# Performance work log

Measured on AMD Instinct MI355X. Metric: run time of the kernel, lower is better.

## Reference

```python
import jax, jax.numpy as jnp
import numpy as np

DIM, FF, E = 1024, 4096, 8
B, S = 2, 2048


def setup_inputs() -> dict:
    key = jax.random.key(0)
    ks = jax.random.split(key, 7)
    sd = 0.02
    return {
        "x":  jax.random.normal(ks[0], (B, S, DIM), dtype=jnp.float32),
        "Wg": jax.random.normal(ks[1], (DIM, E), dtype=jnp.float32) * sd,
        "bg": jnp.zeros((E,), dtype=jnp.float32),
        "W1": jax.random.normal(ks[2], (E, DIM, FF), dtype=jnp.float32) * sd,
        "b1": jnp.zeros((E, FF), dtype=jnp.float32),
        "W2": jax.random.normal(ks[3], (E, FF, DIM), dtype=jnp.float32) * sd,
        "b2": jnp.zeros((E, DIM), dtype=jnp.float32),
    }


def reference(x, Wg, bg, W1, b1, W2, b2):
    # Gate: (B,S,E) softmax over experts
    probs = jax.nn.softmax(x @ Wg + bg, axis=-1)
    # Dense all-expert FFN (matches torch.stack over all experts), dropout is identity (eval)
    h = jax.nn.relu(jnp.einsum("bsd,edf->bsef", x, W1) + b1)        # (B,S,E,FF)
    all_out = jnp.einsum("bsef,efd->bsed", h, W2) + b2               # (B,S,E,DIM)
    # Top-2 routing, renormalized weights
    top_vals, top_idx = jax.lax.top_k(probs, 2)                      # (B,S,2)
    weights = top_vals / (jnp.sum(top_vals, axis=-1, keepdims=True) + 1e-9)
    selected = jnp.take_along_axis(all_out, top_idx[..., None], axis=2)  # (B,S,2,DIM)
    return jnp.sum(selected * weights[..., None], axis=2)            # (B,S,DIM)
```

## Files before the change

kernel.cpp:

```cpp
#include <hip/hip_runtime.h>
#include <hip/hip_bf16.h>


typedef __attribute__((ext_vector_type(8))) short bf16x8;
typedef __attribute__((ext_vector_type(4))) float f32x4;

#define MFMA16(a, b, c) __builtin_amdgcn_mfma_f32_16x16x32_bf16((a), (b), (c), 0, 0, 0)

__device__ __forceinline__ unsigned short f2bf(float f) {
  unsigned u = __builtin_bit_cast(unsigned, f);
  u += 0x7FFFu + ((u >> 16) & 1u);
  return (unsigned short)(u >> 16);
}

__device__ __forceinline__ float bf2f(unsigned short s) {
  return __builtin_bit_cast(float, (unsigned)s << 16);
}

__device__ __forceinline__ void gload_lds16(const void* g, void* l) {
  __builtin_amdgcn_global_load_lds(
      (const __attribute__((address_space(1))) unsigned int*)g,
      (__attribute__((address_space(3))) unsigned int*)l, 16, 0, 0);
}

__device__ __forceinline__ bf16x8 ldsr128(const void* p) {
  bf16x8 r;
  unsigned a = (unsigned)(unsigned long long)p;
  asm volatile("ds_read_b128 %0, %1" : "=v"(r) : "v"(a));
  return r;
}

__global__ __launch_bounds__(256) void gate_kernel(
    const float* __restrict__ x, const float* __restrict__ Wg,
    const float* __restrict__ bg, int* __restrict__ tok_e,
    float* __restrict__ tok_w, unsigned short* __restrict__ xb) {
  const int wave = threadIdx.x >> 6;
  const int lane = threadIdx.x & 63;
  const int t = blockIdx.x * 4 + wave;
  const float* xr = x + (size_t)t * 1024;
  unsigned short* xrow = xb + (size_t)t * 1024;
  double acc[8] = {0, 0, 0, 0, 0, 0, 0, 0};
  for (int i = 0; i < 16; ++i) {
    const int d = i * 64 + lane;
    const float vx = xr[d];
    xrow[d] = f2bf(vx);
    const double xv = (double)vx;
    const float* wr = Wg + d * 8;
#pragma unroll
    for (int e = 0; e < 8; ++e) acc[e] += xv * (double)wr[e];
  }
#pragma unroll
  for (int e = 0; e < 8; ++e) {
    double v = acc[e];
#pragma unroll
    for (int off = 32; off > 0; off >>= 1) v += __shfl_xor(v, off, 64);
    acc[e] = v + (double)bg[e];
  }
  if (lane == 0) {
    int e0 = 0;
#pragma unroll
    for (int e = 1; e < 8; ++e)
      if (acc[e] > acc[e0]) e0 = e;
    int e1 = (e0 == 0) ? 1 : 0;
#pragma unroll
    for (int e = 0; e < 8; ++e) {
      if (e != e0 && acc[e] > acc[e1]) e1 = e;
    }
    const double m = acc[e0];
    double s = 0.0;
#pragma unroll
    for (int e = 0; e < 8; ++e) s += exp(acc[e] - m);
    const double p0 = exp(acc[e0] - m) / s;
    const double p1 = exp(acc[e1] - m) / s;
    const double den = p0 + p1 + 1e-9;
    tok_e[2 * t] = e0;
    tok_e[2 * t + 1] = e1;
    tok_w[2 * t] = (float)(p0 / den);
    tok_w[2 * t + 1] = (float)(p1 / den);
  }
}

__global__ __launch_bounds__(256) void scan_scatter_kernel(
    const int* __restrict__ tok_e, int* __restrict__ counts,
    int* __restrict__ offsets, int* __restrict__ pair_token,
    int* __restrict__ tok_slot) {
  __shared__ int scnt[8];
  __shared__ int scur[8];
  const int tid = threadIdx.x;
  if (tid < 8) scnt[tid] = 0;
  __syncthreads();
  for (int i = tid; i < 8192; i += 256) atomicAdd(&scnt[tok_e[i]], 1);
  __syncthreads();
  if (tid == 0) {
    int s = 0;
    for (int e = 0; e < 8; ++e) {
      counts[e] = scnt[e];
      offsets[e] = s;
      scur[e] = s;
      s += scnt[e];
    }
  }
  __syncthreads();
  for (int t = tid; t < 4096; t += 256) {
#pragma unroll
    for (int j = 0; j < 2; ++j) {
      const int e = tok_e[2 * t + j];
      const int slot = atomicAdd(&scur[e], 1);
      pair_token[slot] = t;
      tok_slot[2 * t + j] = slot;
    }
  }
}

__global__ __launch_bounds__(256) void transW_kernel(
    const float* __restrict__ W1, const float* __restrict__ W2,
    unsigned short* __restrict__ W1t, unsigned short* __restrict__ W2t, int FC,
    int f0, int nW1) {
  __shared__ __align__(16) unsigned short T[64][520];
  const int tid = threadIdx.x;
  const int qi = (tid & 15) * 4;
  const int qo = (tid >> 4) * 4;

  const float* src;
  size_t srcStride;
  unsigned short* dstBase;
  size_t dstStride;

  const int bid = blockIdx.x;
  if (bid < nW1) {
    const int nf = FC / 64;
    const int e = bid / (2 * nf);
    const int rem = bid % (2 * nf);
    const int fb = (rem % nf) * 64;
    const int kb = (rem / nf) * 512;
    src = W1 + ((size_t)e * 1024 + kb) * 4096 + f0 + fb + qi;
    srcStride = 4096;
    dstBase = W1t + ((size_t)e * FC + fb) * 1024 + kb;
    dstStride = 1024;
  } else {
    const int jd = bid - nW1;
    const int nf = FC / 512;
    const int e = jd / (16 * nf);
    const int rem = jd % (16 * nf);
    const int db = (rem % 16) * 64;
    const int fbl = (rem / 16) * 512;
    src = W2 + ((size_t)e * 4096 + f0 + fbl) * 1024 + db + qi;
    srcStride = 1024;
    dstBase = W2t + ((size_t)e * 1024 + db) * FC + fbl;
    dstStride = FC;
  }

#pragma unroll
  for (int it = 0; it < 8; ++it) {
    const int o0 = it * 64 + qo;
    const float* s = src + (size_t)o0 * srcStride;
    const float4 r0 = *(const float4*)s;
    const float4 r1 = *(const float4*)(s + srcStride);
    const float4 r2 = *(const float4*)(s + 2 * srcStride);
    const float4 r3 = *(const float4*)(s + 3 * srcStride);
    uint2 u;
    u.x = (unsigned)f2bf(r0.x) | ((unsigned)f2bf(r1.x) << 16);
    u.y = (unsigned)f2bf(r2.x) | ((unsigned)f2bf(r3.x) << 16);
    *(uint2*)&T[qi + 0][o0] = u;
    u.x = (unsigned)f2bf(r0.y) | ((unsigned)f2bf(r1.y) << 16);
    u.y = (unsigned)f2bf(r2.y) | ((unsigned)f2bf(r3.y) << 16);
    *(uint2*)&T[qi + 1][o0] = u;
    u.x = (unsigned)f2bf(r0.z) | ((unsigned)f2bf(r1.z) << 16);
    u.y = (unsigned)f2bf(r2.z) | ((unsigned)f2bf(r3.z) << 16);
    *(uint2*)&T[qi + 2][o0] = u;
    u.x = (unsigned)f2bf(r0.w) | ((unsigned)f2bf(r1.w) << 16);
    u.y = (unsigned)f2bf(r2.w) | ((unsigned)f2bf(r3.w) << 16);
    *(uint2*)&T[qi + 3][o0] = u;
  }
  __syncthreads();
  const int rr = tid >> 2;
  const int sg = tid & 3;
  unsigned short* dst = dstBase + (size_t)rr * dstStride;
#pragma unroll
  for (int j = 0; j < 16; ++j) {
    const int c = sg + j * 4;
    *(uint4*)(dst + c * 8) = *(const uint4*)&T[rr][c * 8];
  }
}

#define COMPUTE_BODY(ALDS, BLDS)                                          \
  {                                                                       \
    bf16x8 af[4], bfr[4];                                                 \
    af[0] = ldsr128(&ALDS[rdA[0]]);                                       \
    bfr[0] = ldsr128(&BLDS[rdB[0]]);                                      \
    af[1] = ldsr128(&ALDS[rdA[1]]);                                       \
    bfr[1] = ldsr128(&BLDS[rdB[1]]);                                      \
    af[2] = ldsr128(&ALDS[rdA[2]]);                                       \
    bfr[2] = ldsr128(&BLDS[rdB[2]]);                                      \
    af[3] = ldsr128(&ALDS[rdA[3]]);                                       \
    bfr[3] = ldsr128(&BLDS[rdB[3]]);                                      \
    asm volatile("s_waitcnt lgkmcnt(6)" ::: "memory");                    \
    __builtin_amdgcn_sched_barrier(0);                                    \
    acc[0][0] = MFMA16(af[0], bfr[0], acc[0][0]);                         \
    __builtin_amdgcn_sched_barrier(0);                                    \
    asm volatile("s_waitcnt lgkmcnt(4)" ::: "memory");                    \
    __builtin_amdgcn_sched_barrier(0);                                    \
    acc[0][1] = MFMA16(af[0], bfr[1], acc[0][1]);                         \
    acc[1][0] = MFMA16(af[1], bfr[0], acc[1][0]);                         \
    acc[1][1] = MFMA16(af[1], bfr[1], acc[1][1]);                         \
    __builtin_amdgcn_sched_barrier(0);                                    \
    asm volatile("s_waitcnt lgkmcnt(2)" ::: "memory");                    \
    __builtin_amdgcn_sched_barrier(0);                                    \
    acc[0][2] = MFMA16(af[0], bfr[2], acc[0][2]);                         \
    acc[1][2] = MFMA16(af[1], bfr[2], acc[1][2]);                         \
    acc[2][0] = MFMA16(af[2], bfr[0], acc[2][0]);                         \
    acc[2][1] = MFMA16(af[2], bfr[1], acc[2][1]);                         \
    acc[2][2] = MFMA16(af[2], bfr[2], acc[2][2]);                         \
    __builtin_amdgcn_sched_barrier(0);                                    \
    asm volatile("s_waitcnt lgkmcnt(0)" ::: "memory");                    \
    __builtin_amdgcn_sched_barrier(0);                                    \
    acc[0][3] = MFMA16(af[0], bfr[3], acc[0][3]);                         \
    acc[1][3] = MFMA16(af[1], bfr[3], acc[1][3]);                         \
    acc[2][3] = MFMA16(af[2], bfr[3], acc[2][3]);                         \
    acc[3][0] = MFMA16(af[3], bfr[0], acc[3][0]);                         \
    acc[3][1] = MFMA16(af[3], bfr[1], acc[3][1]);                         \
    acc[3][2] = MFMA16(af[3], bfr[2], acc[3][2]);                         \
    acc[3][3] = MFMA16(af[3], bfr[3], acc[3][3]);                         \
    __builtin_amdgcn_sched_barrier(0);                                    \
  }

__global__ __launch_bounds__(256) void gemm1_kernel(
    const unsigned short* __restrict__ xb,
    const unsigned short* __restrict__ W1t, const float* __restrict__ b1,
    const int* __restrict__ counts, const int* __restrict__ offsets,
    const int* __restrict__ pair_token, unsigned short* __restrict__ H, int FC,
    int f0, int NT) {
  const int bid = blockIdx.x;
  const int e = bid & 7;
  const int lid = bid >> 3;
  const int n0 = (lid % NT) * 128;
  const int m0 = (lid / NT) * 128;
  const int count = counts[e];
  if (m0 >= count) return;
  const int offset = offsets[e];

  __shared__ __align__(16) unsigned short Alds[2][128 * 32];
  __shared__ __align__(16) unsigned short Blds[2][128 * 32];
  __shared__ int toklds[128];

  const int tid = threadIdx.x;
  if (tid < 128) {
    int r = m0 + tid;
    if (r >= count) r = count - 1;
    toklds[tid] = pair_token[offset + r];
  }
  __syncthreads();

  const int lane = tid & 63;
  const int wave = tid >> 6;
  const int srow = lane >> 2;
  const int kc = lane & 3;
  const unsigned short* aga[2];
  const unsigned short* bga[2];
  int ldso[2];
#pragma unroll
  for (int i = 0; i < 2; ++i) {
    const int ar = wave * 32 + i * 16 + srow;
    const int xr = (ar >> 1) & 3;
    aga[i] = xb + (size_t)toklds[ar] * 1024 + (kc ^ xr) * 8;
    bga[i] = W1t + ((size_t)e * FC + n0 + ar) * 1024 + (kc ^ xr) * 8;
    ldso[i] = (wave * 32 + i * 16) * 32;
  }

  const int wm = (wave >> 1) * 64;
  const int wn = (wave & 1) * 64;
  const int l16 = lane & 15;
  const int lk = lane >> 4;
  int rdA[4], rdB[4];
#pragma unroll
  for (int mi = 0; mi < 4; ++mi) {
    const int row = wm + mi * 16 + l16;
    rdA[mi] = row * 32 + ((lk ^ ((row >> 1) & 3)) << 3);
  }
#pragma unroll
  for (int nj = 0; nj < 4; ++nj) {
    const int f = wn + nj * 16 + l16;
    rdB[nj] = f * 32 + ((lk ^ ((f >> 1) & 3)) << 3);
  }

  f32x4 acc[4][4] = {};

  auto STAGE = [&](int kt, int buf) {
#pragma unroll
    for (int i = 0; i < 2; ++i) {
      gload_lds16(aga[i] + kt, &Alds[buf][ldso[i]]);
      gload_lds16(bga[i] + kt, &Blds[buf][ldso[i]]);
    }
  };

  const int NTk = 32;
  STAGE(0, 0);
  for (int t = 0; t < NTk; ++t) {
    __builtin_amdgcn_s_barrier();
    if (t + 1 < NTk) {
      STAGE((t + 1) * 32, (t + 1) & 1);
      asm volatile("s_waitcnt vmcnt(4)" ::: "memory");
    } else {
      asm volatile("s_waitcnt vmcnt(0)" ::: "memory");
    }
    __builtin_amdgcn_s_barrier();
    __builtin_amdgcn_sched_barrier(0);
    COMPUTE_BODY(Alds[t & 1], Blds[t & 1]);
  }

#pragma unroll
  for (int mi = 0; mi < 4; ++mi) {
#pragma unroll
    for (int r = 0; r < 4; ++r) {
      const int rl = m0 + wm + mi * 16 + lk * 4 + r;
      if (rl >= count) continue;
      unsigned short* hrow = H + (size_t)(offset + rl) * FC;
#pragma unroll
      for (int nj = 0; nj < 4; ++nj) {
        const int c = n0 + wn + nj * 16 + l16;
        float v = acc[mi][nj][r] + b1[e * 4096 + f0 + c];
        hrow[c] = f2bf(v > 0.f ? v : 0.f);
      }
    }
  }
}

__global__ __launch_bounds__(256) void gemm2_kernel(
    const unsigned short* __restrict__ H,
    const unsigned short* __restrict__ W2t, const float* __restrict__ b2,
    const int* __restrict__ counts, const int* __restrict__ offsets,
    unsigned short* __restrict__ P, int FC, int firstChunk) {
  const int bid = blockIdx.x;
  const int e = bid & 7;
  const int r2 = bid >> 3;
  const int n0 = (r2 & 7) * 128;
  const int m0 = (r2 >> 3) * 128;
  const int count = counts[e];
  if (m0 >= count) return;
  const int offset = offsets[e];

  __shared__ __align__(16) unsigned short Alds[2][128 * 32];
  __shared__ __align__(16) unsigned short Blds[2][128 * 32];

  const int tid = threadIdx.x;
  const int lane = tid & 63;
  const int wave = tid >> 6;
  const int srow = lane >> 2;
  const int kc = lane & 3;
  const unsigned short* aga[2];
  const unsigned short* bga[2];
  int ldso[2];
#pragma unroll
  for (int i = 0; i < 2; ++i) {
    const int tr = wave * 32 + i * 16 + srow;
    int ar = m0 + tr;
    if (ar >= count) ar = count - 1;
    const int xr = (tr >> 1) & 3;
    aga[i] = H + (size_t)(offset + ar) * FC + (kc ^ xr) * 8;
    bga[i] = W2t + ((size_t)e * 1024 + n0 + tr) * FC + (kc ^ xr) * 8;
    ldso[i] = (wave * 32 + i * 16) * 32;
  }

  const int wm = (wave >> 1) * 64;
  const int wn = (wave & 1) * 64;
  const int l16 = lane & 15;
  const int lk = lane >> 4;
  int rdA[4], rdB[4];
#pragma unroll
  for (int mi = 0; mi < 4; ++mi) {
    const int row = wm + mi * 16 + l16;
    rdA[mi] = row * 32 + ((lk ^ ((row >> 1) & 3)) << 3);
  }
#pragma unroll
  for (int nj = 0; nj < 4; ++nj) {
    const int f = wn + nj * 16 + l16;
    rdB[nj] = f * 32 + ((lk ^ ((f >> 1) & 3)) << 3);
  }

  f32x4 acc[4][4] = {};

  auto STAGE = [&](int kt, int buf) {
#pragma unroll
    for (int i = 0; i < 2; ++i) {
      gload_lds16(aga[i] + kt, &Alds[buf][ldso[i]]);
      gload_lds16(bga[i] + kt, &Blds[buf][ldso[i]]);
    }
  };

  const int NTk = FC / 32;
  STAGE(0, 0);
  for (int t = 0; t < NTk; ++t) {
    __builtin_amdgcn_s_barrier();
    if (t + 1 < NTk) {
      STAGE((t + 1) * 32, (t + 1) & 1);
      asm volatile("s_waitcnt vmcnt(4)" ::: "memory");
    } else {
      asm volatile("s_waitcnt vmcnt(0)" ::: "memory");
    }
    __builtin_amdgcn_s_barrier();
    __builtin_amdgcn_sched_barrier(0);
    COMPUTE_BODY(Alds[t & 1], Blds[t & 1]);
  }

#pragma unroll
  for (int mi = 0; mi < 4; ++mi) {
#pragma unroll
    for (int r = 0; r < 4; ++r) {
      const int rl = m0 + wm + mi * 16 + lk * 4 + r;
      if (rl >= count) continue;
      unsigned short* prow = P + (size_t)(offset + rl) * 1024;
#pragma unroll
      for (int nj = 0; nj < 4; ++nj) {
        const int c = n0 + wn + nj * 16 + l16;
        float v = acc[mi][nj][r];
        if (firstChunk) {
          prow[c] = f2bf(v + b2[e * 1024 + c]);
        } else {
          prow[c] = f2bf(bf2f(prow[c]) + v);
        }
      }
    }
  }
}

__global__ __launch_bounds__(256) void combine_kernel(
    const unsigned short* __restrict__ P, const int* __restrict__ tok_slot,
    const float* __restrict__ tok_w, float* __restrict__ out) {
  const int t = blockIdx.x;
  const int d = threadIdx.x * 4;
  const int s0 = tok_slot[2 * t];
  const int s1 = tok_slot[2 * t + 1];
  const float w0 = tok_w[2 * t];
  const float w1 = tok_w[2 * t + 1];
  const ushort4 a = *(const ushort4*)&P[(size_t)s0 * 1024 + d];
  const ushort4 b = *(const ushort4*)&P[(size_t)s1 * 1024 + d];
  float4 r;
  r.x = w0 * bf2f(a.x) + w1 * bf2f(b.x);
  r.y = w0 * bf2f(a.y) + w1 * bf2f(b.y);
  r.z = w0 * bf2f(a.z) + w1 * bf2f(b.z);
  r.w = w0 * bf2f(a.w) + w1 * bf2f(b.w);
  *(float4*)&out[(size_t)t * 1024 + d] = r;
}

extern "C" void kernel_launch(void* const* d_in, const int* in_sizes, int n_in,
                              void* d_out, int out_size, void* d_ws,
                              size_t ws_size, hipStream_t stream) {
  const float* x = (const float*)d_in[0];
  const float* Wg = (const float*)d_in[1];
  const float* bg = (const float*)d_in[2];
  const float* W1 = (const float*)d_in[3];
  const float* b1 = (const float*)d_in[4];
  const float* W2 = (const float*)d_in[5];
  const float* b2 = (const float*)d_in[6];
  float* out = (float*)d_out;

  char* w = (char*)d_ws;
  int* counts = (int*)w;
  int* offsets = counts + 16;
  int* tok_e = (int*)(w + 1024);
  float* tok_w = (float*)(w + 1024 + 32768);
  int* pair_token = (int*)(w + 1024 + 65536);
  int* tok_slot = (int*)(w + 1024 + 98304);
  unsigned short* xb = (unsigned short*)(w + 256 * 1024);
  unsigned short* P =
      (unsigned short*)(w + 256 * 1024 + 8 * 1024 * 1024);
  char* big = w + 256 * 1024 + 8 * 1024 * 1024 + 16 * 1024 * 1024;
  const size_t avail =
      ws_size - (256 * 1024 + 8 * 1024 * 1024 + 16 * 1024 * 1024);

  int FC = 4096;
  while (FC > 512 && (size_t)FC * 49152 > avail) FC >>= 1;

  unsigned short* W1t = (unsigned short*)big;
  unsigned short* W2t = W1t + (size_t)8 * FC * 1024;
  unsigned short* Hc = W2t + (size_t)8 * 1024 * FC;

  gate_kernel<<<1024, 256, 0, stream>>>(x, Wg, bg, tok_e, tok_w, xb);
  scan_scatter_kernel<<<1, 256, 0, stream>>>(tok_e, counts, offsets,
                                             pair_token, tok_slot);

  const int NT = FC / 128;
  const int nW1 = (FC / 64) * 2 * 8;
  const int nW2 = 16 * (FC / 512) * 8;
  for (int f0 = 0; f0 < 4096; f0 += FC) {
    transW_kernel<<<nW1 + nW2, 256, 0, stream>>>(W1, W2, W1t, W2t, FC, f0,
                                                 nW1);
    gemm1_kernel<<<8 * 32 * NT, 256, 0, stream>>>(
        xb, W1t, b1, counts, offsets, pair_token, Hc, FC, f0, NT);
    gemm2_kernel<<<8 * 8 * 32, 256, 0, stream>>>(
        Hc, W2t, b2, counts, offsets, P, FC, f0 == 0 ? 1 : 0);
  }
  combine_kernel<<<4096, 256, 0, stream>>>(P, tok_slot, tok_w, out);
}
```

Baseline: 340.9 us.

## Double K-tile depth to 64 in both expert GEMMs with 8-way XOR swizzle

Both grouped GEMM kernels now stage a K-slice of 64 instead of 32 per iteration. Each thread issues four 16-byte global-to-LDS loads per operand, and the XOR swizzle of the LDS layout is rewritten for 64-element rows. This halves the number of barriers and loop iterations per tile and puts 32 MFMAs between syncs. In exchange, LDS use doubles to about 64KB per block, which may reduce occupancy, and the finer-grained waits that interleaved LDS reads with MFMAs are replaced by two coarse waits.

```diff
diff --git a/kernel.cpp b/kernel.cpp
--- a/kernel.cpp
+++ b/kernel.cpp
@@ -183,44 +183,36 @@
   }
 }
 
-#define COMPUTE_BODY(ALDS, BLDS)                                          \
+#define COMPUTE64(ALDS, BLDS)                                             \
   {                                                                       \
-    bf16x8 af[4], bfr[4];                                                 \
-    af[0] = ldsr128(&ALDS[rdA[0]]);                                       \
-    bfr[0] = ldsr128(&BLDS[rdB[0]]);                                      \
-    af[1] = ldsr128(&ALDS[rdA[1]]);                                       \
-    bfr[1] = ldsr128(&BLDS[rdB[1]]);                                      \
-    af[2] = ldsr128(&ALDS[rdA[2]]);                                       \
-    bfr[2] = ldsr128(&BLDS[rdB[2]]);                                      \
-    af[3] = ldsr128(&ALDS[rdA[3]]);                                       \
-    bfr[3] = ldsr128(&BLDS[rdB[3]]);                                      \
-    asm volatile("s_waitcnt lgkmcnt(6)" ::: "memory");                    \
+    bf16x8 a0[4], b0[4], a1[4], b1[4];                                    \
+    a0[0] = ldsr128(&ALDS[rdA[0][0]]);                                    \
+    a0[1] = ldsr128(&ALDS[rdA[0][1]]);                                    \
+    a0[2] = ldsr128(&ALDS[rdA[0][2]]);                                    \
+    a0[3] = ldsr128(&ALDS[rdA[0][3]]);                                    \
+    b0[0] = ldsr128(&BLDS[rdB[0][0]]);                                    \
+    b0[1] = ldsr128(&BLDS[rdB[0][1]]);                                    \
+    b0[2] = ldsr128(&BLDS[rdB[0][2]]);                                    \
+    b0[3] = ldsr128(&BLDS[rdB[0][3]]);                                    \
+    a1[0] = ldsr128(&ALDS[rdA[1][0]]);                                    \
+    a1[1] = ldsr128(&ALDS[rdA[1][1]]);                                    \
+    a1[2] = ldsr128(&ALDS[rdA[1][2]]);                                    \
+    a1[3] = ldsr128(&ALDS[rdA[1][3]]);                                    \
+    b1[0] = ldsr128(&BLDS[rdB[1][0]]);                                    \
+    b1[1] = ldsr128(&BLDS[rdB[1][1]]);                                    \
+    b1[2] = ldsr128(&BLDS[rdB[1][2]]);                                    \
+    b1[3] = ldsr128(&BLDS[rdB[1][3]]);                                    \
+    asm volatile("s_waitcnt lgkmcnt(8)" ::: "memory");                    \
     __builtin_amdgcn_sched_barrier(0);                                    \
-    acc[0][0] = MFMA16(af[0], bfr[0], acc[0][0]);                         \
-    __builtin_amdgcn_sched_barrier(0);                                    \
-    asm volatile("s_waitcnt lgkmcnt(4)" ::: "memory");                    \
-    __builtin_amdgcn_sched_barrier(0);                                    \
-    acc[0][1] = MFMA16(af[0], bfr[1], acc[0][1]);                         \
-    acc[1][0] = MFMA16(af[1], bfr[0], acc[1][0]);                         \
-    acc[1][1] = MFMA16(af[1], bfr[1], acc[1][1]);                         \
-    __builtin_amdgcn_sched_barrier(0);                                    \
-    asm volatile("s_waitcnt lgkmcnt(2)" ::: "memory");                    \
-    __builtin_amdgcn_sched_barrier(0);                                    \
-    acc[0][2] = MFMA16(af[0], bfr[2], acc[0][2]);                         \
-    acc[1][2] = MFMA16(af[1], bfr[2], acc[1][2]);                         \
-    acc[2][0] = MFMA16(af[2], bfr[0], acc[2][0]);                         \
-    acc[2][1] = MFMA16(af[2], bfr[1], acc[2][1]);                         \
-    acc[2][2] = MFMA16(af[2], bfr[2], acc[2][2]);                         \
+    _Pragma("unroll") for (int mi = 0; mi < 4; ++mi)                      \
+        _Pragma("unroll") for (int nj = 0; nj < 4; ++nj)                  \
+        acc[mi][nj] = MFMA16(a0[mi], b0[nj], acc[mi][nj]);                \
     __builtin_amdgcn_sched_barrier(0);                                    \
     asm volatile("s_waitcnt lgkmcnt(0)" ::: "memory");                    \
     __builtin_amdgcn_sched_barrier(0);                                    \
-    acc[0][3] = MFMA16(af[0], bfr[3], acc[0][3]);                         \
-    acc[1][3] = MFMA16(af[1], bfr[3], acc[1][3]);                         \
-    acc[2][3] = MFMA16(af[2], bfr[3], acc[2][3]);                         \
-    acc[3][0] = MFMA16(af[3], bfr[0], acc[3][0]);                         \
-    acc[3][1] = MFMA16(af[3], bfr[1], acc[3][1]);                         \
-    acc[3][2] = MFMA16(af[3], bfr[2], acc[3][2]);                         \
-    acc[3][3] = MFMA16(af[3], bfr[3], acc[3][3]);                         \
+    _Pragma("unroll") for (int mi = 0; mi < 4; ++mi)                      \
+        _Pragma("unroll") for (int nj = 0; nj < 4; ++nj)                  \
+        acc[mi][nj] = MFMA16(a1[mi], b1[nj], acc[mi][nj]);                \
     __builtin_amdgcn_sched_barrier(0);                                    \
   }
 
@@ -239,8 +231,8 @@
   if (m0 >= count) return;
   const int offset = offsets[e];
 
-  __shared__ __align__(16) unsigned short Alds[2][128 * 32];
-  __shared__ __align__(16) unsigned short Blds[2][128 * 32];
+  __shared__ __align__(16) unsigned short Alds[2][128 * 64];
+  __shared__ __align__(16) unsigned short Blds[2][128 * 64];
   __shared__ int toklds[128];
 
   const int tid = threadIdx.x;
@@ -253,59 +245,62 @@
 
   const int lane = tid & 63;
   const int wave = tid >> 6;
-  const int srow = lane >> 2;
-  const int kc = lane & 3;
-  const unsigned short* aga[2];
-  const unsigned short* bga[2];
-  int ldso[2];
-#pragma unroll
-  for (int i = 0; i < 2; ++i) {
-    const int ar = wave * 32 + i * 16 + srow;
-    const int xr = (ar >> 1) & 3;
-    aga[i] = xb + (size_t)toklds[ar] * 1024 + (kc ^ xr) * 8;
-    bga[i] = W1t + ((size_t)e * FC + n0 + ar) * 1024 + (kc ^ xr) * 8;
-    ldso[i] = (wave * 32 + i * 16) * 32;
+
+  const unsigned short* agp[4];
+  const unsigned short* bgp[4];
+  int ldso[4];
+#pragma unroll
+  for (int j = 0; j < 4; ++j) {
+    const int g = tid + 256 * j;
+    const int row = g >> 3;
+    const int c = g & 7;
+    const int sc = c ^ (row & 7);
+    agp[j] = xb + (size_t)toklds[row] * 1024 + sc * 8;
+    bgp[j] = W1t + ((size_t)e * FC + n0 + row) * 1024 + sc * 8;
+    ldso[j] = (wave * 64 + 256 * j) * 8;
   }
 
   const int wm = (wave >> 1) * 64;
   const int wn = (wave & 1) * 64;
   const int l16 = lane & 15;
   const int lk = lane >> 4;
-  int rdA[4], rdB[4];
-#pragma unroll
-  for (int mi = 0; mi < 4; ++mi) {
-    const int row = wm + mi * 16 + l16;
-    rdA[mi] = row * 32 + ((lk ^ ((row >> 1) & 3)) << 3);
-  }
-#pragma unroll
-  for (int nj = 0; nj < 4; ++nj) {
-    const int f = wn + nj * 16 + l16;
-    rdB[nj] = f * 32 + ((lk ^ ((f >> 1) & 3)) << 3);
+  int rdA[2][4], rdB[2][4];
+#pragma unroll
+  for (int h = 0; h < 2; ++h) {
+#pragma unroll
+    for (int mi = 0; mi < 4; ++mi) {
+      const int row = wm + mi * 16 + l16;
+      rdA[h][mi] = row * 64 + (((h * 4 + lk) ^ (row & 7)) << 3);
+    }
+#pragma unroll
+    for (int nj = 0; nj < 4; ++nj) {
+      const int row = wn + nj * 16 + l16;
+      rdB[h][nj] = row * 64 + (((h * 4 + lk) ^ (row & 7)) << 3);
+    }
   }
 
   f32x4 acc[4][4] = {};
 
   auto STAGE = [&](int kt, int buf) {
 #pragma unroll
-    for (int i = 0; i < 2; ++i) {
-      gload_lds16(aga[i] + kt, &Alds[buf][ldso[i]]);
-      gload_lds16(bga[i] + kt, &Blds[buf][ldso[i]]);
-    }
+    for (int j = 0; j < 4; ++j) gload_lds16(agp[j] + kt * 64, &Alds[buf][ldso[j]]);
+#pragma unroll
+    for (int j = 0; j < 4; ++j) gload_lds16(bgp[j] + kt * 64, &Blds[buf][ldso[j]]);
   };
 
-  const int NTk = 32;
+  const int NTk = 16;
   STAGE(0, 0);
   for (int t = 0; t < NTk; ++t) {
     __builtin_amdgcn_s_barrier();
     if (t + 1 < NTk) {
-      STAGE((t + 1) * 32, (t + 1) & 1);
-      asm volatile("s_waitcnt vmcnt(4)" ::: "memory");
+      STAGE(t + 1, (t + 1) & 1);
+      asm volatile("s_waitcnt vmcnt(8)" ::: "memory");
     } else {
       asm volatile("s_waitcnt vmcnt(0)" ::: "memory");
     }
     __builtin_amdgcn_s_barrier();
     __builtin_amdgcn_sched_barrier(0);
-    COMPUTE_BODY(Alds[t & 1], Blds[t & 1]);
+    COMPUTE64(Alds[t & 1], Blds[t & 1]);
   }
 
 #pragma unroll
@@ -339,67 +334,70 @@
   if (m0 >= count) return;
   const int offset = offsets[e];
 
-  __shared__ __align__(16) unsigned short Alds[2][128 * 32];
-  __shared__ __align__(16) unsigned short Blds[2][128 * 32];
+  __shared__ __align__(16) unsigned short Alds[2][128 * 64];
+  __shared__ __align__(16) unsigned short Blds[2][128 * 64];
 
   const int tid = threadIdx.x;
   const int lane = tid & 63;
   const int wave = tid >> 6;
-  const int srow = lane >> 2;
-  const int kc = lane & 3;
-  const unsigned short* aga[2];
-  const unsigned short* bga[2];
-  int ldso[2];
-#pragma unroll
-  for (int i = 0; i < 2; ++i) {
-    const int tr = wave * 32 + i * 16 + srow;
-    int ar = m0 + tr;
+
+  const unsigned short* agp[4];
+  const unsigned short* bgp[4];
+  int ldso[4];
+#pragma unroll
+  for (int j = 0; j < 4; ++j) {
+    const int g = tid + 256 * j;
+    const int row = g >> 3;
+    const int c = g & 7;
+    const int sc = c ^ (row & 7);
+    int ar = m0 + row;
     if (ar >= count) ar = count - 1;
-    const int xr = (tr >> 1) & 3;
-    aga[i] = H + (size_t)(offset + ar) * FC + (kc ^ xr) * 8;
-    bga[i] = W2t + ((size_t)e * 1024 + n0 + tr) * FC + (kc ^ xr) * 8;
-    ldso[i] = (wave * 32 + i * 16) * 32;
+    agp[j] = H + (size_t)(offset + ar) * FC + sc * 8;
+    bgp[j] = W2t + ((size_t)e * 1024 + n0 + row) * FC + sc * 8;
+    ldso[j] = (wave * 64 + 256 * j) * 8;
   }
 
   const int wm = (wave >> 1) * 64;
   const int wn = (wave & 1) * 64;
   const int l16 = lane & 15;
   const int lk = lane >> 4;
-  int rdA[4], rdB[4];
-#pragma unroll
-  for (int mi = 0; mi < 4; ++mi) {
-    const int row = wm + mi * 16 + l16;
-    rdA[mi] = row * 32 + ((lk ^ ((row >> 1) & 3)) << 3);
-  }
-#pragma unroll
-  for (int nj = 0; nj < 4; ++nj) {
-    const int f = wn + nj * 16 + l16;
-    rdB[nj] = f * 32 + ((lk ^ ((f >> 1) & 3)) << 3);
+  int rdA[2][4], rdB[2][4];
+#pragma unroll
+  for (int h = 0; h < 2; ++h) {
+#pragma unroll
+    for (int mi = 0; mi < 4; ++mi) {
+      const int row = wm + mi * 16 + l16;
+      rdA[h][mi] = row * 64 + (((h * 4 + lk) ^ (row & 7)) << 3);
+    }
+#pragma unroll
+    for (int nj = 0; nj < 4; ++nj) {
+      const int row = wn + nj * 16 + l16;
+      rdB[h][nj] = row * 64 + (((h * 4 + lk) ^ (row & 7)) << 3);
+    }
   }
 
   f32x4 acc[4][4] = {};
 
   auto STAGE = [&](int kt, int buf) {
 #pragma unroll
-    for (int i = 0; i < 2; ++i) {
-      gload_lds16(aga[i] + kt, &Alds[buf][ldso[i]]);
-      gload_lds16(bga[i] + kt, &Blds[buf][ldso[i]]);
-    }
+    for (int j = 0; j < 4; ++j) gload_lds16(agp[j] + kt * 64, &Alds[buf][ldso[j]]);
+#pragma unroll
+    for (int j = 0; j < 4; ++j) gload_lds16(bgp[j] + kt * 64, &Blds[buf][ldso[j]]);
   };
 
-  const int NTk = FC / 32;
+  const int NTk = FC / 64;
   STAGE(0, 0);
   for (int t = 0; t < NTk; ++t) {
     __builtin_amdgcn_s_barrier();
     if (t + 1 < NTk) {
-      STAGE((t + 1) * 32, (t + 1) & 1);
-      asm volatile("s_waitcnt vmcnt(4)" ::: "memory");
+      STAGE(t + 1, (t + 1) & 1);
+      asm volatile("s_waitcnt vmcnt(8)" ::: "memory");
     } else {
       asm volatile("s_waitcnt vmcnt(0)" ::: "memory");
     }
     __builtin_amdgcn_s_barrier();
     __builtin_amdgcn_sched_barrier(0);
-    COMPUTE_BODY(Alds[t & 1], Blds[t & 1]);
+    COMPUTE64(Alds[t & 1], Blds[t & 1]);
   }
 
 #pragma unroll
```

Result: faster. 333.3 us (-2.2%).
